# Optimization experiments

Hardware: AMD Instinct MI355X
Metric: run time of the kernel (lower is better)

The kernel has to match this reference:

```python
import jax, jax.numpy as jnp
import numpy as np

B, S, D = 2, 2048, 2048
H, KV, HD = 32, 8, 64
REP = H // KV
THETA = 10000.0


def _rope_tables(seq_len, head_dim, dtype):
    inv_freq = 1.0 / (THETA ** (jnp.arange(0, head_dim, 2, dtype=jnp.float32) / head_dim))
    t = jnp.arange(seq_len, dtype=jnp.float32)
    freqs = jnp.outer(t, inv_freq)  # [S, HD/2]
    return jnp.cos(freqs).astype(dtype), jnp.sin(freqs).astype(dtype)


def _apply_rope(x, cos, sin):
    # x: [B, S, nh, HD]; cos/sin: [S, HD/2] -> broadcast [1, S, 1, HD/2]
    c = cos[None, :, None, :]
    s = sin[None, :, None, :]
    x1, x2 = x[..., : HD // 2], x[..., HD // 2:]
    return jnp.concatenate([x1 * c - x2 * s, x1 * s + x2 * c], axis=-1)


def setup_inputs() -> dict:
    key = jax.random.key(0)
    ks = jax.random.split(key, 5)
    x = jax.random.normal(ks[0], (B, S, D), dtype=jnp.float32)
    wq = jax.random.normal(ks[1], (D, H * HD), dtype=jnp.float32) * 0.02
    wk = jax.random.normal(ks[2], (D, KV * HD), dtype=jnp.float32) * 0.02
    wv = jax.random.normal(ks[3], (D, KV * HD), dtype=jnp.float32) * 0.02
    wo = jax.random.normal(ks[4], (H * HD, D), dtype=jnp.float32) * 0.02
    return {"x": x, "wq": wq, "wk": wk, "wv": wv, "wo": wo}


def reference(x, wq, wk, wv, wo):
    b, s, _ = x.shape
    q = (x @ wq).reshape(b, s, H, HD)
    k = (x @ wk).reshape(b, s, KV, HD)
    v = (x @ wv).reshape(b, s, KV, HD)

    cos, sin = _rope_tables(s, HD, x.dtype)
    q = _apply_rope(q, cos, sin)
    k = _apply_rope(k, cos, sin)

    # GQA: group query heads by KV head instead of repeating K/V (same math).
    qg = q.reshape(b, s, KV, REP, HD)  # [B,S,G,R,HD]
    scale = HD ** -0.5
    # scores: [B, G, R, Sq, Sk]
    scores = jnp.einsum("bsgrd,btgd->bgrst", qg, k) * scale
    causal = jnp.tril(jnp.ones((s, s), dtype=bool))
    scores = jnp.where(causal[None, None, None], scores, jnp.finfo(scores.dtype).min)
    probs = jax.nn.softmax(scores, axis=-1)
    out = jnp.einsum("bgrst,btgd->bsgrd", probs, v)  # [B,S,G,R,HD]
    out = out.reshape(b, s, H * HD)
    return out @ wo
```

## Files before the change

kernel.cpp:

```cpp
#include <hip/hip_runtime.h>

#define S_LEN 2048
#define NH 32
#define NKV 8
#define HEADD 64
#define DMODEL 2048
#define NQKV 3072

typedef float f32x4 __attribute__((ext_vector_type(4)));
typedef float f32x16 __attribute__((ext_vector_type(16)));
typedef short s16x8 __attribute__((ext_vector_type(8)));
typedef int   i32x4 __attribute__((ext_vector_type(4)));
typedef unsigned short u16;
typedef u16 u16x4 __attribute__((ext_vector_type(4)));

__device__ __forceinline__ float b2f(u16 u) {
  unsigned int x = ((unsigned int)u) << 16;
  float f;
  __builtin_memcpy(&f, &x, 4);
  return f;
}
__device__ __forceinline__ u16 f2b(float f) {
  unsigned int x;
  __builtin_memcpy(&x, &f, 4);
  unsigned int r = x + 0x7fffu + ((x >> 16) & 1u);
  return (u16)(r >> 16);
}
__device__ __forceinline__ unsigned fbits(float f) {
  unsigned x; __builtin_memcpy(&x, &f, 4); return x;
}

__device__ __forceinline__ void gload_lds16(const u16* g, u16* l) {
  __builtin_amdgcn_global_load_lds((const __attribute__((address_space(1))) void*)g,
                                   (__attribute__((address_space(3))) void*)l, 16, 0, 0);
}

template<int N> __device__ __forceinline__ void wait_vm() {
  asm volatile("s_waitcnt vmcnt(%0)" :: "n"(N) : "memory");
}

__global__ void cast_x_kernel(const float* __restrict__ src, u16* __restrict__ dst) {
  int i = (blockIdx.x * 256 + threadIdx.x) * 4;
  f32x4 v = *(const f32x4*)(src + i);
  u16x4 o;
  o[0] = f2b(v[0]); o[1] = f2b(v[1]); o[2] = f2b(v[2]); o[3] = f2b(v[3]);
  *(u16x4*)(dst + i) = o;
}

__global__ void transpose_cast(const float* __restrict__ src, u16* __restrict__ dst, int N, int K) {
  __shared__ float tile[32][33];
  int n0 = blockIdx.x * 32, k0 = blockIdx.y * 32;
  int tx = threadIdx.x, ty = threadIdx.y;
#pragma unroll
  for (int i = 0; i < 32; i += 8)
    tile[ty + i][tx] = src[(size_t)(k0 + ty + i) * N + n0 + tx];
  __syncthreads();
#pragma unroll
  for (int i = 0; i < 32; i += 8)
    dst[(size_t)(n0 + ty + i) * K + k0 + tx] = f2b(tile[tx][ty + i]);
}

#define PIPE_BODY(Q, STAGE, VMN)                                                   \
  {                                                                                \
    wait_vm<VMN>();                                                                \
    __builtin_amdgcn_s_barrier();                                                  \
    __builtin_amdgcn_sched_barrier(0);                                             \
    if (STAGE) {                                                                   \
      u16* db = sm + ((Q + 3) & 3) * BUFE;                                         \
      gload_lds16(gA0, db + w * 1024);                                             \
      gload_lds16(gA1, db + w * 1024 + 512);                                       \
      if (BN == 256) {                                                             \
        gload_lds16(gB0, db + ABUF + w * 1024);                                    \
        gload_lds16(gB1, db + ABUF + w * 1024 + 512);                              \
      } else {                                                                     \
        gload_lds16(gB0, db + ABUF + w * 512);                                     \
      }                                                                            \
      gA0 += 32; gA1 += 32; gB0 += 32; if (BN == 256) gB1 += 32;                   \
    }                                                                              \
    const u16* bb = sm + Q * BUFE;                                                 \
    s16x8 af[8], bf[NF];                                                           \
    _Pragma("unroll") for (int i = 0; i < 8; i++)  af[i] = *(const s16x8*)(bb + aoff[i]); \
    _Pragma("unroll") for (int j = 0; j < NF; j++) bf[j] = *(const s16x8*)(bb + boff[j]); \
    __builtin_amdgcn_s_setprio(1);                                                 \
    _Pragma("unroll") for (int mi = 0; mi < 8; mi++)                               \
      _Pragma("unroll") for (int ni = 0; ni < NF; ni++)                            \
        acc[mi][ni] = __builtin_amdgcn_mfma_f32_16x16x32_bf16(af[mi], bf[ni], acc[mi][ni], 0, 0, 0); \
    __builtin_amdgcn_s_setprio(0);                                                 \
  }

template<int BN>
__global__ __launch_bounds__(512, 2) void gemm_pipe(
    const u16* __restrict__ A, const u16* __restrict__ Bt, void* __restrict__ Cout,
    int M, int N, int writeF32) {
  extern __shared__ __align__(16) u16 sm[];
  constexpr int NF   = BN / 64;
  constexpr int ABUF = 256 * 32;
  constexpr int BUFE = ABUF + BN * 32;
  constexpr int LPS  = 2 + BN / 128;

  int nb = N / BN;
  int nwg = (M >> 8) * nb;
  int cpx = nwg >> 3;
  int bid = ((int)blockIdx.x & 7) * cpx + ((int)blockIdx.x >> 3);
  int m0 = (bid / nb) << 8;
  int n0 = (bid % nb) * BN;

  int tid = threadIdx.x;
  int lane = tid & 63;
  int w = tid >> 6;
  int wm8 = (w >> 2) << 7;
  int wn8 = (w & 3) * (BN / 4);
  int l15 = lane & 15;
  int quad = lane >> 4;

  int lr = lane >> 3;
  int lc = lane & 7;
  int slot = lc ^ lr;
  int kc8 = (slot & 3) << 3;
  const u16* gA0 = A + (size_t)(m0 + w * 32 + (lr << 1) + (slot >> 2)) * 2048 + kc8;
  const u16* gA1 = gA0 + (size_t)16 * 2048;
  const u16* gB0;
  const u16* gB1;
  if (BN == 256) {
    gB0 = Bt + (size_t)(n0 + w * 32 + (lr << 1) + (slot >> 2)) * 2048 + kc8;
    gB1 = gB0 + (size_t)16 * 2048;
  } else {
    gB0 = Bt + (size_t)(n0 + w * 16 + (lr << 1) + (slot >> 2)) * 2048 + kc8;
    gB1 = gB0;
  }

  int rb = l15 >> 1;
  int sl = (((((l15 & 1) << 2) | quad) ^ rb)) << 3;
  int rbase = rb * 64 + sl;
  int aoff[8], boff[NF];
#pragma unroll
  for (int i = 0; i < 8; i++) aoff[i] = wm8 * 32 + i * 512 + rbase;
#pragma unroll
  for (int j = 0; j < NF; j++) boff[j] = ABUF + wn8 * 32 + j * 512 + rbase;

  f32x4 acc[8][NF] = {};

#pragma unroll
  for (int pt = 0; pt < 3; pt++) {
    u16* db = sm + pt * BUFE;
    gload_lds16(gA0, db + w * 1024);
    gload_lds16(gA1, db + w * 1024 + 512);
    if (BN == 256) {
      gload_lds16(gB0, db + ABUF + w * 1024);
      gload_lds16(gB1, db + ABUF + w * 1024 + 512);
    } else {
      gload_lds16(gB0, db + ABUF + w * 512);
    }
    gA0 += 32; gA1 += 32; gB0 += 32; if (BN == 256) gB1 += 32;
  }

#pragma unroll 1
  for (int it = 0; it < 15; ++it) {
    PIPE_BODY(0, 1, 2 * LPS)
    PIPE_BODY(1, 1, 2 * LPS)
    PIPE_BODY(2, 1, 2 * LPS)
    PIPE_BODY(3, 1, 2 * LPS)
  }
  PIPE_BODY(0, 1, 2 * LPS)
  PIPE_BODY(1, 0, 2 * LPS)
  PIPE_BODY(2, 0, LPS)
  PIPE_BODY(3, 0, 0)

#pragma unroll
  for (int mi = 0; mi < 8; mi++)
#pragma unroll
    for (int ni = 0; ni < NF; ni++)
#pragma unroll
      for (int r = 0; r < 4; r++) {
        int row = m0 + wm8 + mi * 16 + (quad << 2) + r;
        int col = n0 + wn8 + ni * 16 + l15;
        float v = acc[mi][ni][r];
        if (writeF32) ((float*)Cout)[(size_t)row * N + col] = v;
        else ((u16*)Cout)[(size_t)row * N + col] = f2b(v);
      }
}

__global__ void rope_kernel(u16* __restrict__ qkv) {
  __shared__ float cs_s[32], sn_s[32];
  int row = blockIdx.x;
  int s = row & (S_LEN - 1);
  u16* p = qkv + (size_t)row * NQKV;
  int t = threadIdx.x;
  int d = t & 31;
  int hh = t >> 5;
  if (t < 32) {
    float inv_freq = exp2f(-(float)t * (13.287712379549449f / 32.0f));
    float ang = (float)s * inv_freq;
    float sn, cs;
    sincosf(ang, &sn, &cs);
    cs_s[t] = cs;
    sn_s[t] = sn;
  }
  __syncthreads();
  float cs = cs_s[d], sn = sn_s[d];
  const float QSCALE = 0.18033688011112042f;
#pragma unroll
  for (int i = 0; i < 4; i++) {
    int base = (hh + (i << 3)) * HEADD + d;
    float x1 = b2f(p[base]);
    float x2 = b2f(p[base + 32]);
    p[base]      = f2b((x1 * cs - x2 * sn) * QSCALE);
    p[base + 32] = f2b((x1 * sn + x2 * cs) * QSCALE);
  }
  {
    int base = DMODEL + hh * HEADD + d;
    float x1 = b2f(p[base]);
    float x2 = b2f(p[base + 32]);
    p[base]      = f2b(x1 * cs - x2 * sn);
    p[base + 32] = f2b(x1 * sn + x2 * cs);
  }
}

__global__ void vtrans_kernel(const u16* __restrict__ qkv, u16* __restrict__ Vt) {
  __shared__ __align__(16) u16 tile[64][72];
  int bid = blockIdx.x;
  int st = bid & 31;
  int g  = (bid >> 5) & 7;
  int b  = bid >> 8;
  int tid = threadIdx.x;
  int r = tid >> 2;
  int c = (tid & 3) << 4;
  const u16* src = qkv + (size_t)(b * S_LEN + st * 64 + r) * NQKV + 2560 + g * 64 + c;
  *(i32x4*)&tile[r][c]     = *(const i32x4*)src;
  *(i32x4*)&tile[r][c + 8] = *(const i32x4*)(src + 8);
  __syncthreads();
  u16* dst = Vt + (size_t)((b * 8 + g) * 64 + r) * S_LEN + st * 64 + c;
  u16 tmp[16];
#pragma unroll
  for (int j = 0; j < 16; j++) tmp[j] = tile[c + j][r];
  *(i32x4*)dst       = *(i32x4*)&tmp[0];
  *(i32x4*)(dst + 8) = *(i32x4*)&tmp[8];
}

__global__ __launch_bounds__(64) void kvpack_kernel(const u16* __restrict__ qkv,
                                                    const u16* __restrict__ Vt,
                                                    u16* __restrict__ Kp,
                                                    u16* __restrict__ Vp) {
  int bid = blockIdx.x;
  int kb = bid & 63;
  int bg = bid >> 6;
  int g = bg & 7;
  int b = bg >> 3;
  int lane = threadIdx.x;
  int l31 = lane & 31;
  int h2 = lane >> 5;

  const u16* kq = qkv + (size_t)(b * S_LEN + kb * 32 + l31) * NQKV + DMODEL + g * 64 + h2 * 8;
  u16* kdst = Kp + ((size_t)bid * 4) * 512 + lane * 8;
#pragma unroll
  for (int t = 0; t < 4; t++)
    *(i32x4*)(kdst + t * 512) = *(const i32x4*)(kq + t * 16);

  const u16* vq = Vt + (size_t)(bg * 64 + l31) * S_LEN + kb * 32 + h2 * 8;
  u16* vdst = Vp + ((size_t)bid * 4) * 512 + lane * 8;
  *(i32x4*)(vdst)        = *(const i32x4*)vq;
  *(i32x4*)(vdst + 512)  = *(const i32x4*)(vq + 16);
  *(i32x4*)(vdst + 1024) = *(const i32x4*)(vq + (size_t)32 * S_LEN);
  *(i32x4*)(vdst + 1536) = *(const i32x4*)(vq + (size_t)32 * S_LEN + 16);
}

__global__ __launch_bounds__(64) void attn_kernel(const u16* __restrict__ qkv,
                                                  const u16* __restrict__ Kp,
                                                  const u16* __restrict__ Vp,
                                                  u16* __restrict__ out) {
  int bid = blockIdx.x;
  int bh = bid & 63;
  int qb = 63 - (bid >> 6);
  int h = bh & 31;
  int b = bh >> 5;
  int g = h >> 2;
  int bg = b * 8 + g;
  int lane = threadIdx.x;
  int l31 = lane & 31;
  int h2 = lane >> 5;
  int q0 = qb << 5;

  const u16* qp = qkv + (size_t)(b * S_LEN + q0 + l31) * NQKV + h * HEADD + h2 * 8;
  s16x8 qf[4];
#pragma unroll
  for (int t = 0; t < 4; t++) qf[t] = *(const s16x8*)(qp + t * 16);

  const u16* kp = Kp + ((size_t)bg * 64) * 2048 + lane * 8;
  const u16* vp = Vp + ((size_t)bg * 64) * 2048 + lane * 8;

  float l_i = 0.f;
  f32x16 acc[2] = {};

  s16x8 kfa[4], vfa[4], kfb[4], vfb[4];

  auto loadkv = [&](int kb, s16x8 (&kf)[4], s16x8 (&vf)[4]) {
    const u16* kpp = kp + (size_t)kb * 2048;
    const u16* vpp = vp + (size_t)kb * 2048;
#pragma unroll
    for (int t = 0; t < 4; t++) {
      kf[t] = *(const s16x8*)(kpp + t * 512);
      vf[t] = *(const s16x8*)(vpp + t * 512);
    }
  };

  auto compute = [&](int kb, s16x8 (&kf)[4], s16x8 (&vf)[4]) {
    f32x16 sc = {};
    __builtin_amdgcn_s_setprio(1);
#pragma unroll
    for (int t = 0; t < 4; t++)
      sc = __builtin_amdgcn_mfma_f32_32x32x16_bf16(kf[t], qf[t], sc, 0, 0, 0);
    __builtin_amdgcn_s_setprio(0);

    float sv[16];
#pragma unroll
    for (int j = 0; j < 16; j++) sv[j] = sc[j];

    if (kb == qb) {
      int qg = q0 + l31;
#pragma unroll
      for (int j = 0; j < 16; j++) {
        int kg = kb * 32 + (j & 3) + ((j >> 2) << 3) + (h2 << 2);
        if (kg > qg) sv[j] = -1e30f;
      }
    }

    float e[16];
#pragma unroll
    for (int j = 0; j < 16; j++) e[j] = __builtin_amdgcn_exp2f(sv[j]);

    float ps = (((e[0] + e[1]) + (e[2] + e[3])) + ((e[4] + e[5]) + (e[6] + e[7])))
             + (((e[8] + e[9]) + (e[10] + e[11])) + ((e[12] + e[13]) + (e[14] + e[15])));
    ps += __shfl_xor(ps, 32);
    l_i += ps;

    unsigned Pk[8], Ex[8];
#pragma unroll
    for (int r = 0; r < 8; r++) {
      unsigned pk;
      asm("v_cvt_pk_bf16_f32 %0, %1, %2" : "=v"(pk) : "v"(e[2 * r]), "v"(e[2 * r + 1]));
      Pk[r] = pk;
    }
#pragma unroll
    for (int r = 0; r < 8; r++) Ex[r] = (unsigned)__shfl_xor((int)Pk[r], 32);

    unsigned B0u[4], B1u[4];
    B0u[0] = h2 ? Ex[2] : Pk[0];
    B0u[1] = h2 ? Ex[3] : Pk[1];
    B0u[2] = h2 ? Pk[2] : Ex[0];
    B0u[3] = h2 ? Pk[3] : Ex[1];
    B1u[0] = h2 ? Ex[6] : Pk[4];
    B1u[1] = h2 ? Ex[7] : Pk[5];
    B1u[2] = h2 ? Pk[6] : Ex[4];
    B1u[3] = h2 ? Pk[7] : Ex[5];
    s16x8 B0, B1;
    __builtin_memcpy(&B0, B0u, 16);
    __builtin_memcpy(&B1, B1u, 16);

    __builtin_amdgcn_s_setprio(1);
    acc[0] = __builtin_amdgcn_mfma_f32_32x32x16_bf16(vf[0], B0, acc[0], 0, 0, 0);
    acc[0] = __builtin_amdgcn_mfma_f32_32x32x16_bf16(vf[1], B1, acc[0], 0, 0, 0);
    acc[1] = __builtin_amdgcn_mfma_f32_32x32x16_bf16(vf[2], B0, acc[1], 0, 0, 0);
    acc[1] = __builtin_amdgcn_mfma_f32_32x32x16_bf16(vf[3], B1, acc[1], 0, 0, 0);
    __builtin_amdgcn_s_setprio(0);
  };

  loadkv(0, kfa, vfa);
  int kb = 0;
  while (true) {
    if (kb < qb) loadkv(kb + 1, kfb, vfb);
    compute(kb, kfa, vfa);
    if (++kb > qb) break;
    if (kb < qb) loadkv(kb + 1, kfa, vfa);
    compute(kb, kfb, vfb);
    if (++kb > qb) break;
  }

  float linv = 1.0f / l_i;
  u16* op = out + (size_t)(b * S_LEN + q0 + l31) * DMODEL + h * HEADD;
#pragma unroll
  for (int dt = 0; dt < 2; dt++)
#pragma unroll
    for (int rg = 0; rg < 4; rg++) {
      u16x4 t4;
#pragma unroll
      for (int j = 0; j < 4; j++) t4[j] = f2b(acc[dt][rg * 4 + j] * linv);
      *(u16x4*)(op + dt * 32 + rg * 8 + h2 * 4) = t4;
    }
}

extern "C" void kernel_launch(void* const* d_in, const int* in_sizes, int n_in,
                              void* d_out, int out_size, void* d_ws, size_t ws_size,
                              hipStream_t stream) {
  const float* x  = (const float*)d_in[0];
  const float* wq = (const float*)d_in[1];
  const float* wk = (const float*)d_in[2];
  const float* wv = (const float*)d_in[3];
  const float* wo = (const float*)d_in[4];

  char* ws = (char*)d_ws;
  u16* xb    = (u16*)ws;
  u16* wqkvT = (u16*)(ws + 16777216);
  u16* woT   = (u16*)(ws + 16777216 + 12582912);
  u16* qkv   = (u16*)(ws + 16777216 + 12582912 + 8388608);
  u16* attnb = xb;
  u16* Vt    = wqkvT;
  u16* Kp    = (u16*)(ws + 16777216 + 4194304);
  u16* Vp    = (u16*)(ws + 16777216 + 8388608);

  hipFuncSetAttribute(reinterpret_cast<const void*>(gemm_pipe<256>),
                      hipFuncAttributeMaxDynamicSharedMemorySize, 131072);
  hipFuncSetAttribute(reinterpret_cast<const void*>(gemm_pipe<128>),
                      hipFuncAttributeMaxDynamicSharedMemorySize, 98304);

  cast_x_kernel<<<8192, 256, 0, stream>>>(x, xb);
  dim3 tb(32, 8);
  transpose_cast<<<dim3(64, 64), tb, 0, stream>>>(wq, wqkvT, 2048, 2048);
  transpose_cast<<<dim3(16, 64), tb, 0, stream>>>(wk, wqkvT + (size_t)2048 * 2048, 512, 2048);
  transpose_cast<<<dim3(16, 64), tb, 0, stream>>>(wv, wqkvT + (size_t)2560 * 2048, 512, 2048);
  transpose_cast<<<dim3(64, 64), tb, 0, stream>>>(wo, woT, 2048, 2048);

  gemm_pipe<256><<<192, 512, 131072, stream>>>(xb, wqkvT, qkv, 4096, NQKV, 0);
  rope_kernel<<<4096, 256, 0, stream>>>(qkv);
  vtrans_kernel<<<512, 256, 0, stream>>>(qkv, Vt);
  kvpack_kernel<<<1024, 64, 0, stream>>>(qkv, Vt, Kp, Vp);
  attn_kernel<<<4096, 64, 0, stream>>>(qkv, Kp, Vp, attnb);
  gemm_pipe<128><<<256, 512, 98304, stream>>>(attnb, woT, d_out, 4096, 2048, 1);
}
```

Before: 285.9 us.

## Share K/V tiles across GQA heads via LDS with multi-stage async pipeline

The attention kernel now runs one 256-thread block per (batch, KV group, query tile), with four waves each handling one of the four query heads that share the KV group. K/V tiles are staged once into a 4-deep LDS ring buffer via direct global-to-LDS loads and read by all four waves, instead of each head's wave loading its own copy from global memory into registers. This cuts redundant global K/V traffic at the cost of block-wide barriers per tile and LDS usage. The RoPE kernel is also changed to vectorized 4-element loads and stores with 320 threads per row.

```diff
diff --git a/kernel.cpp b/kernel.cpp
--- a/kernel.cpp
+++ b/kernel.cpp
@@ -186,8 +186,6 @@
   int s = row & (S_LEN - 1);
   u16* p = qkv + (size_t)row * NQKV;
   int t = threadIdx.x;
-  int d = t & 31;
-  int hh = t >> 5;
   if (t < 32) {
     float inv_freq = exp2f(-(float)t * (13.287712379549449f / 32.0f));
     float ang = (float)s * inv_freq;
@@ -197,23 +195,23 @@
     sn_s[t] = sn;
   }
   __syncthreads();
-  float cs = cs_s[d], sn = sn_s[d];
   const float QSCALE = 0.18033688011112042f;
-#pragma unroll
-  for (int i = 0; i < 4; i++) {
-    int base = (hh + (i << 3)) * HEADD + d;
-    float x1 = b2f(p[base]);
-    float x2 = b2f(p[base + 32]);
-    p[base]      = f2b((x1 * cs - x2 * sn) * QSCALE);
-    p[base + 32] = f2b((x1 * sn + x2 * cs) * QSCALE);
-  }
-  {
-    int base = DMODEL + hh * HEADD + d;
-    float x1 = b2f(p[base]);
-    float x2 = b2f(p[base + 32]);
-    p[base]      = f2b(x1 * cs - x2 * sn);
-    p[base + 32] = f2b(x1 * sn + x2 * cs);
-  }
+  int hu = t >> 3;
+  int j = t & 7;
+  int off = (hu < 32) ? hu * HEADD + j * 4 : DMODEL + (hu - 32) * HEADD + j * 4;
+  float scale = (hu < 32) ? QSCALE : 1.0f;
+  u16x4 a = *(const u16x4*)(p + off);
+  u16x4 c = *(const u16x4*)(p + off + 32);
+  u16x4 o1, o2;
+#pragma unroll
+  for (int jj = 0; jj < 4; jj++) {
+    float x1 = b2f(a[jj]), x2 = b2f(c[jj]);
+    float cs = cs_s[j * 4 + jj], sn = sn_s[j * 4 + jj];
+    o1[jj] = f2b((x1 * cs - x2 * sn) * scale);
+    o2[jj] = f2b((x1 * sn + x2 * cs) * scale);
+  }
+  *(u16x4*)(p + off) = o1;
+  *(u16x4*)(p + off + 32) = o2;
 }
 
 __global__ void vtrans_kernel(const u16* __restrict__ qkv, u16* __restrict__ Vt) {
@@ -264,62 +262,78 @@
   *(i32x4*)(vdst + 1536) = *(const i32x4*)(vq + (size_t)32 * S_LEN + 16);
 }
 
-__global__ __launch_bounds__(64) void attn_kernel(const u16* __restrict__ qkv,
-                                                  const u16* __restrict__ Kp,
-                                                  const u16* __restrict__ Vp,
-                                                  u16* __restrict__ out) {
+#define ASTEP(T, STG, VMN)                                                         \
+  {                                                                                \
+    wait_vm<VMN>();                                                                \
+    __builtin_amdgcn_s_barrier();                                                  \
+    __builtin_amdgcn_sched_barrier(0);                                             \
+    if (STG) {                                                                     \
+      int skb = (T) + 3;                                                           \
+      u16* db = &kvbuf[((T) + 3) & 3][wv * 512];                                   \
+      gload_lds16(kSrc + (size_t)skb * 2048, db);                                  \
+      gload_lds16(vSrc + (size_t)skb * 2048, db + 2048);                           \
+    }                                                                              \
+    compute_t(T);                                                                  \
+  }
+
+__global__ __launch_bounds__(256) void attn_kernel(const u16* __restrict__ qkv,
+                                                   const u16* __restrict__ Kp,
+                                                   const u16* __restrict__ Vp,
+                                                   u16* __restrict__ out) {
+  __shared__ __align__(16) u16 kvbuf[4][4096];
+
   int bid = blockIdx.x;
-  int bh = bid & 63;
-  int qb = 63 - (bid >> 6);
-  int h = bh & 31;
-  int b = bh >> 5;
-  int g = h >> 2;
-  int bg = b * 8 + g;
-  int lane = threadIdx.x;
+  int bg16 = bid & 15;
+  int qb = 63 - (bid >> 4);
+  int g = bg16 & 7;
+  int b = bg16 >> 3;
+  int tid = threadIdx.x;
+  int wv = tid >> 6;
+  int lane = tid & 63;
   int l31 = lane & 31;
   int h2 = lane >> 5;
+  int h = g * 4 + wv;
   int q0 = qb << 5;
+  int nt = qb + 1;
 
   const u16* qp = qkv + (size_t)(b * S_LEN + q0 + l31) * NQKV + h * HEADD + h2 * 8;
   s16x8 qf[4];
 #pragma unroll
   for (int t = 0; t < 4; t++) qf[t] = *(const s16x8*)(qp + t * 16);
 
-  const u16* kp = Kp + ((size_t)bg * 64) * 2048 + lane * 8;
-  const u16* vp = Vp + ((size_t)bg * 64) * 2048 + lane * 8;
+  const u16* kSrc = Kp + ((size_t)bg16 * 64) * 2048 + wv * 512 + lane * 8;
+  const u16* vSrc = Vp + ((size_t)bg16 * 64) * 2048 + wv * 512 + lane * 8;
 
   float l_i = 0.f;
   f32x16 acc[2] = {};
 
-  s16x8 kfa[4], vfa[4], kfb[4], vfb[4];
-
-  auto loadkv = [&](int kb, s16x8 (&kf)[4], s16x8 (&vf)[4]) {
-    const u16* kpp = kp + (size_t)kb * 2048;
-    const u16* vpp = vp + (size_t)kb * 2048;
-#pragma unroll
-    for (int t = 0; t < 4; t++) {
-      kf[t] = *(const s16x8*)(kpp + t * 512);
-      vf[t] = *(const s16x8*)(vpp + t * 512);
-    }
-  };
-
-  auto compute = [&](int kb, s16x8 (&kf)[4], s16x8 (&vf)[4]) {
+  auto compute_t = [&](int T) {
+    const u16* bb = &kvbuf[T & 3][0];
+    s16x8 kf[4], vf[4];
+#pragma unroll
+    for (int tt = 0; tt < 4; tt++)
+      kf[tt] = *(const s16x8*)(bb + tt * 512 + lane * 8);
+
     f32x16 sc = {};
     __builtin_amdgcn_s_setprio(1);
 #pragma unroll
-    for (int t = 0; t < 4; t++)
-      sc = __builtin_amdgcn_mfma_f32_32x32x16_bf16(kf[t], qf[t], sc, 0, 0, 0);
+    for (int tt = 0; tt < 4; tt++)
+      sc = __builtin_amdgcn_mfma_f32_32x32x16_bf16(kf[tt], qf[tt], sc, 0, 0, 0);
     __builtin_amdgcn_s_setprio(0);
 
+#pragma unroll
+    for (int tt = 0; tt < 4; tt++)
+      vf[tt] = *(const s16x8*)(bb + 2048 + tt * 512 + lane * 8);
+
     float sv[16];
 #pragma unroll
     for (int j = 0; j < 16; j++) sv[j] = sc[j];
 
-    if (kb == qb) {
+    if (T == qb) {
       int qg = q0 + l31;
 #pragma unroll
       for (int j = 0; j < 16; j++) {
-        int kg = kb * 32 + (j & 3) + ((j >> 2) << 3) + (h2 << 2);
+        int kg = qb * 32 + (j & 3) + ((j >> 2) << 3) + (h2 << 2);
         if (kg > qg) sv[j] = -1e30f;
       }
     }
@@ -364,16 +378,22 @@
     __builtin_amdgcn_s_setprio(0);
   };
 
-  loadkv(0, kfa, vfa);
-  int kb = 0;
-  while (true) {
-    if (kb < qb) loadkv(kb + 1, kfb, vfb);
-    compute(kb, kfa, vfa);
-    if (++kb > qb) break;
-    if (kb < qb) loadkv(kb + 1, kfa, vfa);
-    compute(kb, kfb, vfb);
-    if (++kb > qb) break;
-  }
+#pragma unroll
+  for (int pt = 0; pt < 3; ++pt) {
+    int skb = pt < nt ? pt : (nt - 1);
+    u16* db = &kvbuf[pt][wv * 512];
+    gload_lds16(kSrc + (size_t)skb * 2048, db);
+    gload_lds16(vSrc + (size_t)skb * 2048, db + 2048);
+  }
+
+  int t = 0;
+#pragma unroll 1
+  for (; t + 3 < nt; ++t) ASTEP(t, 1, 4)
+  ASTEP(t, 0, 4); ++t;
+  if (t < nt) { ASTEP(t, 0, 2); ++t; }
+  if (t < nt) { ASTEP(t, 0, 0); }
+
+  wait_vm<0>();
 
   float linv = 1.0f / l_i;
   u16* op = out + (size_t)(b * S_LEN + q0 + l31) * DMODEL + h * HEADD;
@@ -420,9 +440,9 @@
   transpose_cast<<<dim3(64, 64), tb, 0, stream>>>(wo, woT, 2048, 2048);
 
   gemm_pipe<256><<<192, 512, 131072, stream>>>(xb, wqkvT, qkv, 4096, NQKV, 0);
-  rope_kernel<<<4096, 256, 0, stream>>>(qkv);
+  rope_kernel<<<4096, 320, 0, stream>>>(qkv);
   vtrans_kernel<<<512, 256, 0, stream>>>(qkv, Vt);
   kvpack_kernel<<<1024, 64, 0, stream>>>(qkv, Vt, Kp, Vp);
-  attn_kernel<<<4096, 64, 0, stream>>>(qkv, Kp, Vp, attnb);
+  attn_kernel<<<1024, 256, 0, stream>>>(qkv, Kp, Vp, attnb);
   gemm_pipe<128><<<256, 512, 98304, stream>>>(attnb, woT, d_out, 4096, 2048, 1);
 }
```

New measurement: 281.3 us. No clear change (-1.6%).
